# Optimization experiments

Hardware: AMD Instinct MI355X
Metric: run time of the kernel (lower is better)

Reference implementation:

```python
import jax, jax.numpy as jnp
import numpy as np

N = 50000          # num nodes
EDG = 1600000      # num edges
DIM = 128          # in_dim == out_dim (dim_h)
H = 8              # num_heads
HD = DIM // H      # head dim = 16
BN_EPS = 1e-5


def _batchnorm(x, gamma, beta):
    # training-mode BatchNorm1d: biased batch stats over node axis
    mean = x.mean(axis=0)
    var = x.var(axis=0)
    return (x - mean) * jax.lax.rsqrt(var + BN_EPS) * gamma + beta


def setup_inputs() -> dict:
    key = jax.random.key(0)
    ks = jax.random.split(key, 12)
    lin = lambda k, o, i: jax.random.normal(k, (o, i), jnp.float32) * (1.0 / np.sqrt(i))
    return {
        "h": jax.random.normal(ks[0], (N, DIM), jnp.float32),
        "edge_index": jax.random.randint(ks[1], (2, EDG), 0, N, jnp.int32),
        "edge_attr": jax.random.normal(ks[2], (EDG, DIM), jnp.float32),
        "Wq": lin(ks[3], DIM, DIM),
        "Wk": lin(ks[4], DIM, DIM),
        "Wv": lin(ks[5], DIM, DIM),
        "We": lin(ks[6], DIM, DIM),
        "Wb": lin(ks[7], H, DIM),
        "bb": jnp.zeros((H,), jnp.float32),
        "gamma1": jnp.ones((DIM,), jnp.float32),
        "beta1": jnp.zeros((DIM,), jnp.float32),
        "W1": lin(ks[8], 2 * DIM, DIM),
        "b1": jnp.zeros((2 * DIM,), jnp.float32),
        "W2": lin(ks[9], DIM, 2 * DIM),
        "b2": jnp.zeros((DIM,), jnp.float32),
        "gamma2": jnp.ones((DIM,), jnp.float32),
        "beta2": jnp.zeros((DIM,), jnp.float32),
    }


def reference(h, edge_index, edge_attr, Wq, Wk, Wv, We, Wb, bb,
              gamma1, beta1, W1, b1, W2, b2, gamma2, beta2):
    n = h.shape[0]
    src, dst = edge_index[0], edge_index[1]

    Qh = (h @ Wq.T).reshape(n, H, HD)
    Kh = (h @ Wk.T).reshape(n, H, HD)
    Vh = (h @ Wv.T).reshape(n, H, HD)
    E = (edge_attr @ We.T).reshape(-1, H, HD)          # (EDG, H, HD)
    E_bias = edge_attr @ Wb.T + bb                      # (EDG, H)

    # per-edge attention score: sum over head dim of Kh[src]*Qh[dst]*E
    score = (Kh[src] * Qh[dst] * E).sum(-1) / np.sqrt(HD) + E_bias
    score = jnp.exp(jnp.clip(score, -5.0, 5.0))         # (EDG, H)

    msg = Vh[src] * score[..., None]                    # (EDG, H, HD)
    wV = jax.ops.segment_sum(msg, dst, num_segments=n)  # (N, H, HD)
    Z = jax.ops.segment_sum(score, dst, num_segments=n) # (N, H)

    h_attn = (wV / (Z[..., None] + 1e-6)).reshape(n, DIM)
    x = h + h_attn                                      # residual
    x = _batchnorm(x, gamma1, beta1)

    ff = jax.nn.relu(x @ W1.T + b1) @ W2.T + b2
    out = _batchnorm(x + ff, gamma2, beta2)
    return out
```

## Files before the change

kernel.cpp:

```cpp
#include <hip/hip_runtime.h>
#include <math.h>

typedef __attribute__((ext_vector_type(8))) short bf16x8;
typedef __attribute__((ext_vector_type(4))) short bf16x4;
typedef __attribute__((ext_vector_type(4))) float f32x4;

static __device__ __forceinline__ unsigned short f2bf(float x){
    union{float f; unsigned u;} v; v.f = x;
    unsigned r = v.u + 0x7fffu + ((v.u >> 16) & 1u);
    return (unsigned short)(r >> 16);
}
static __device__ __forceinline__ unsigned cvtpk(float lo, float hi){
    unsigned r;
    asm("v_cvt_pk_bf16_f32 %0, %1, %2" : "=v"(r) : "v"(lo), "v"(hi));
    return r;
}
static __device__ __forceinline__ float bflo(unsigned u){
    union{unsigned x; float f;} v; v.x = u << 16; return v.f;
}
static __device__ __forceinline__ float bfhi(unsigned u){
    union{unsigned x; float f;} v; v.x = u & 0xffff0000u; return v.f;
}

__global__ __launch_bounds__(128)
void qkv_kernel(const float* __restrict__ h,
                const float* __restrict__ Wq, const float* __restrict__ Wk,
                const float* __restrict__ Wv,
                float* __restrict__ Qb, unsigned short* __restrict__ Kb16,
                unsigned short* __restrict__ Vb16)
{
    __shared__ float hl[16 * 128];
    const int t  = threadIdx.x;
    const int n0 = blockIdx.x * 16;

    const float4* hg4 = (const float4*)(h + (size_t)n0 * 128);
    float4* hl4 = (float4*)hl;
    #pragma unroll
    for (int i = 0; i < 4; ++i) hl4[i * 128 + t] = hg4[i * 128 + t];
    __syncthreads();

    #pragma unroll
    for (int m = 0; m < 3; ++m) {
        const float* W = (m == 0 ? Wq : (m == 1 ? Wk : Wv)) + t * 128;
        float acc[16];
        #pragma unroll
        for (int n = 0; n < 16; ++n) acc[n] = 0.f;
        for (int kc = 0; kc < 32; ++kc) {
            const float4 w = *(const float4*)(W + kc * 4);
            #pragma unroll
            for (int n = 0; n < 16; ++n) {
                const float4 x = *(const float4*)&hl[n * 128 + kc * 4];
                acc[n] += w.x * x.x + w.y * x.y + w.z * x.z + w.w * x.w;
            }
        }
        if (m == 0) {
            float* o = Qb + (size_t)n0 * 128 + t;
            #pragma unroll
            for (int n = 0; n < 16; ++n) o[(size_t)n * 128] = acc[n];
        } else {
            unsigned short* o = (m == 1 ? Kb16 : Vb16) + (size_t)n0 * 128 + t;
            #pragma unroll
            for (int n = 0; n < 16; ++n) o[(size_t)n * 128] = f2bf(acc[n]);
        }
    }
}

__global__ void hist_kernel(const int* __restrict__ ei, int* __restrict__ cnt, int EDG)
{
    const int stride = gridDim.x * blockDim.x;
    for (int e = blockIdx.x * blockDim.x + threadIdx.x; e < EDG; e += stride)
        atomicAdd(&cnt[ei[EDG + e]], 1);
}

__global__ __launch_bounds__(1024)
void scan_a(const int* __restrict__ cnt, int* __restrict__ bsum, int n)
{
    __shared__ int tmp[1024];
    const int t = threadIdx.x;
    const int i = blockIdx.x * 1024 + t;
    tmp[t] = (i < n) ? cnt[i] : 0;
    __syncthreads();
    for (int d = 512; d > 0; d >>= 1) {
        if (t < d) tmp[t] += tmp[t + d];
        __syncthreads();
    }
    if (t == 0) bsum[blockIdx.x] = tmp[0];
}

__global__ void scan_b(const int* __restrict__ bsum, int* __restrict__ bbase,
                       int* __restrict__ offs, int nb, int n)
{
    if (threadIdx.x == 0) {
        int run = 0;
        for (int b = 0; b < nb; ++b) { bbase[b] = run; run += bsum[b]; }
        offs[n] = run;
    }
}

__global__ __launch_bounds__(1024)
void scan_c(const int* __restrict__ cnt, const int* __restrict__ bbase,
            int* __restrict__ offs, int n)
{
    __shared__ int tmp[1024];
    const int t = threadIdx.x;
    const int i = blockIdx.x * 1024 + t;
    const int v = (i < n) ? cnt[i] : 0;
    tmp[t] = v;
    __syncthreads();
    for (int d = 1; d < 1024; d <<= 1) {
        const int a = (t >= d) ? tmp[t - d] : 0;
        __syncthreads();
        tmp[t] += a;
        __syncthreads();
    }
    if (i < n) offs[i] = bbase[blockIdx.x] + tmp[t] - v;
}

__global__ void scatter_kernel(const int* __restrict__ ei, const int* __restrict__ offs,
                               int* __restrict__ cnt, int2* __restrict__ elist, int EDG)
{
    const int stride = gridDim.x * blockDim.x;
    for (int e = blockIdx.x * blockDim.x + threadIdx.x; e < EDG; e += stride) {
        const int d = ei[EDG + e];
        const int p = atomicSub(&cnt[d], 1) - 1;
        int2 v; v.x = ei[e]; v.y = e;
        elist[offs[d] + p] = v;
    }
}

__global__ __launch_bounds__(256, 3)
void fused_attn(const float* __restrict__ eattr, const int2* __restrict__ elist,
                const int* __restrict__ offs,
                const float* __restrict__ We, const float* __restrict__ Wb,
                const float* __restrict__ bbv,
                const float* __restrict__ Qb, const unsigned short* __restrict__ Kb16,
                const unsigned short* __restrict__ Vb16, const float* __restrict__ h,
                float* __restrict__ x, float* __restrict__ stat, int N, int EDG)
{
    __shared__ unsigned short WeB[128 * 128];
    __shared__ unsigned short WbB[16 * 128];
    __shared__ float scw[4][16][8];
    __shared__ int   srw[4][16];

    const int t = threadIdx.x;
    #pragma unroll
    for (int i = 0; i < 16; ++i) {
        const int idx4 = i * 256 + t;
        const int d = idx4 >> 5, k0 = (idx4 & 31) * 4;
        const float4 wv = *(const float4*)&We[d * 128 + k0];
        bf16x4 p;
        p[0] = (short)f2bf(wv.x); p[1] = (short)f2bf(wv.y);
        p[2] = (short)f2bf(wv.z); p[3] = (short)f2bf(wv.w);
        *(bf16x4*)((char*)WeB + d * 256 + ((2 * k0) ^ ((d & 7) << 4))) = p;
    }
    #pragma unroll
    for (int i = 0; i < 8; ++i) {
        const int idx = i * 256 + t;
        const int r = idx >> 7, k = idx & 127;
        const unsigned short v = (r < 8) ? f2bf(Wb[r * 128 + k]) : (unsigned short)0;
        *(unsigned short*)((char*)WbB + r * 256 + ((2 * k) ^ ((r & 7) << 4))) = v;
    }
    __syncthreads();

    const int l = t & 63, w = t >> 6;
    const int eloc = l & 15, g4 = l >> 4;
    const int half = l >> 5, q = l & 31;
    const int hq = q >> 2;
    const int kb_l = g4 * 16;
    float bb[8];
    #pragma unroll
    for (int hh = 0; hh < 8; ++hh) bb[hh] = bbv[hh];

    float4 sA = {0.f, 0.f, 0.f, 0.f}, sQ2 = {0.f, 0.f, 0.f, 0.f};
    const int GW = gridDim.x * 4;
    for (int node = blockIdx.x * 4 + w; node < N; node += GW) {
        const int beg = offs[node], end = offs[node + 1];

        const float* qrow = Qb + (size_t)node * 128 + g4 * 4;
        float4 qv[8];
        #pragma unroll
        for (int hh = 0; hh < 8; ++hh) qv[hh] = *(const float4*)(qrow + hh * 16);

        float4 pv = {0.f, 0.f, 0.f, 0.f};
        float zz = 0.f;

        for (int base = beg; base < end; base += 16) {
            const int cnt = min(16, end - base);
            const int ii = min(base + eloc, EDG - 1);
            const int2 se = elist[ii];

            bf16x8 frv[4];
            {
                const float* ep = eattr + (size_t)se.y * 128 + g4 * 8;
                #pragma unroll
                for (int ks = 0; ks < 4; ++ks) {
                    const float4 a0 = *(const float4*)(ep + ks * 32);
                    const float4 a1 = *(const float4*)(ep + ks * 32 + 4);
                    union { unsigned u[4]; bf16x8 v; } fr;
                    fr.u[0] = cvtpk(a0.x, a0.y);
                    fr.u[1] = cvtpk(a0.z, a0.w);
                    fr.u[2] = cvtpk(a1.x, a1.y);
                    fr.u[3] = cvtpk(a1.z, a1.w);
                    frv[ks] = fr.v;
                }
            }
            const unsigned short* kr16 = Kb16 + (size_t)se.x * 128 + g4 * 4;

            f32x4 acc[8], accb;
            #pragma unroll
            for (int hh = 0; hh < 8; ++hh) acc[hh] = (f32x4){0.f, 0.f, 0.f, 0.f};
            accb = (f32x4){0.f, 0.f, 0.f, 0.f};
            #pragma unroll
            for (int ks = 0; ks < 4; ++ks) {
                const int kb = ks * 64 + kb_l;
                const bf16x8 abf = *(const bf16x8*)((char*)WbB + eloc * 256 + (kb ^ ((eloc & 7) << 4)));
                accb = __builtin_amdgcn_mfma_f32_16x16x32_bf16(abf, frv[ks], accb, 0, 0, 0);
                #pragma unroll
                for (int hh = 0; hh < 8; ++hh) {
                    const int ar = hh * 16 + eloc;
                    const bf16x8 af = *(const bf16x8*)((char*)WeB + ar * 256 + (kb ^ ((ar & 7) << 4)));
                    acc[hh] = __builtin_amdgcn_mfma_f32_16x16x32_bf16(af, frv[ks], acc[hh], 0, 0, 0);
                }
            }

            float scv[8];
            #pragma unroll
            for (int hh = 0; hh < 8; ++hh) {
                const uint2  k2 = *(const uint2*)(kr16 + hh * 16);
                const float4 qq = qv[hh];
                float m = acc[hh][0] * (bflo(k2.x) * qq.x)
                        + acc[hh][1] * (bfhi(k2.x) * qq.y)
                        + acc[hh][2] * (bflo(k2.y) * qq.z)
                        + acc[hh][3] * (bfhi(k2.y) * qq.w);
                m += __shfl_xor(m, 16);
                m += __shfl_xor(m, 32);
                const float eb = __shfl(accb[hh & 3], ((hh >> 2) << 4) | eloc);
                float sc = m * 0.25f + eb + bb[hh];
                sc = expf(fminf(fmaxf(sc, -5.f), 5.f));
                scv[hh] = (eloc < cnt) ? sc : 0.f;
            }
            if (l < 16) {
                float4 s0 = {scv[0], scv[1], scv[2], scv[3]};
                float4 s1 = {scv[4], scv[5], scv[6], scv[7]};
                *(float4*)&scw[w][l][0] = s0;
                *(float4*)&scw[w][l][4] = s1;
                srw[w][l] = se.x;
            }
            asm volatile("s_waitcnt lgkmcnt(0)" ::: "memory");
            __builtin_amdgcn_sched_barrier(0);

            int e = half;
            for (; e + 2 < cnt; e += 4) {
                const int   s0 = srw[w][e],     s1 = srw[w][e + 2];
                const float c0 = scw[w][e][hq], c1 = scw[w][e + 2][hq];
                const uint2 u0 = *(const uint2*)(Vb16 + (size_t)s0 * 128 + 4 * q);
                const uint2 u1 = *(const uint2*)(Vb16 + (size_t)s1 * 128 + 4 * q);
                pv.x += bflo(u0.x) * c0 + bflo(u1.x) * c1;
                pv.y += bfhi(u0.x) * c0 + bfhi(u1.x) * c1;
                pv.z += bflo(u0.y) * c0 + bflo(u1.y) * c1;
                pv.w += bfhi(u0.y) * c0 + bfhi(u1.y) * c1;
                zz += c0 + c1;
            }
            for (; e < cnt; e += 2) {
                const int   s0 = srw[w][e];
                const float c0 = scw[w][e][hq];
                const uint2 u0 = *(const uint2*)(Vb16 + (size_t)s0 * 128 + 4 * q);
                pv.x += bflo(u0.x) * c0; pv.y += bfhi(u0.x) * c0;
                pv.z += bflo(u0.y) * c0; pv.w += bfhi(u0.y) * c0;
                zz += c0;
            }
        }

        pv.x += __shfl_xor(pv.x, 32); pv.y += __shfl_xor(pv.y, 32);
        pv.z += __shfl_xor(pv.z, 32); pv.w += __shfl_xor(pv.w, 32);
        zz   += __shfl_xor(zz, 32);
        if (half == 0) {
            const float inv = 1.f / (zz + 1e-6f);
            const float4 hv = *(const float4*)&h[(size_t)node * 128 + 4 * q];
            float4 xv;
            xv.x = hv.x + pv.x * inv; xv.y = hv.y + pv.y * inv;
            xv.z = hv.z + pv.z * inv; xv.w = hv.w + pv.w * inv;
            *(float4*)&x[(size_t)node * 128 + 4 * q] = xv;
            sA.x += xv.x; sA.y += xv.y; sA.z += xv.z; sA.w += xv.w;
            sQ2.x += xv.x * xv.x; sQ2.y += xv.y * xv.y;
            sQ2.z += xv.z * xv.z; sQ2.w += xv.w * xv.w;
        }
    }

    __syncthreads();
    float* wbF = (float*)WbB;
    if (half == 0) {
        *(float4*)&wbF[w * 256 + 4 * q]       = sA;
        *(float4*)&wbF[w * 256 + 128 + 4 * q] = sQ2;
    }
    __syncthreads();
    if (t < 128) {
        float s = 0.f, sq2 = 0.f;
        #pragma unroll
        for (int wi = 0; wi < 4; ++wi) {
            s   += wbF[wi * 256 + t];
            sq2 += wbF[wi * 256 + 128 + t];
        }
        atomicAdd(&stat[t], s);
        atomicAdd(&stat[128 + t], sq2);
    }
}

__global__ void bn_params(const float* __restrict__ sum, const float* __restrict__ sumsq,
                          const float* __restrict__ gamma, const float* __restrict__ beta,
                          float* __restrict__ a, float* __restrict__ b, float invn)
{
    const int c = threadIdx.x;
    const float mean = sum[c] * invn;
    const float var  = sumsq[c] * invn - mean * mean;
    const float sc   = gamma[c] * rsqrtf(var + 1e-5f);
    a[c] = sc;
    b[c] = beta[c] - mean * sc;
}

__global__ __launch_bounds__(128)
void ffn_kernel(const float* __restrict__ x, const float* __restrict__ W1,
                const float* __restrict__ b1, const float* __restrict__ W2,
                const float* __restrict__ b2, const float* __restrict__ par,
                float* __restrict__ zb, float* __restrict__ stat2)
{
    __shared__ float xnl[16 * 128];
    __shared__ float hidl[16 * 256];
    const int t  = threadIdx.x;
    const int n0 = blockIdx.x * 16;

    const float4* xg4 = (const float4*)(x + (size_t)n0 * 128);
    const float4* a4  = (const float4*)par;
    const float4* bv4 = (const float4*)(par + 128);
    float4* xnl4 = (float4*)xnl;
    #pragma unroll
    for (int i = 0; i < 4; ++i) {
        const int idx = i * 128 + t;
        const float4 xv = xg4[idx];
        const float4 av = a4[idx & 31], bv = bv4[idx & 31];
        float4 r;
        r.x = xv.x * av.x + bv.x; r.y = xv.y * av.y + bv.y;
        r.z = xv.z * av.z + bv.z; r.w = xv.w * av.w + bv.w;
        xnl4[idx] = r;
    }
    __syncthreads();

    float acc0[16], acc1[16];
    #pragma unroll
    for (int n = 0; n < 16; ++n) { acc0[n] = 0.f; acc1[n] = 0.f; }
    const float* w0p = W1 + (size_t)t * 128;
    const float* w1p = W1 + (size_t)(t + 128) * 128;
    for (int kc = 0; kc < 32; ++kc) {
        const float4 w0 = *(const float4*)(w0p + kc * 4);
        const float4 w1 = *(const float4*)(w1p + kc * 4);
        #pragma unroll
        for (int n = 0; n < 16; ++n) {
            const float4 xv = *(const float4*)&xnl[n * 128 + kc * 4];
            acc0[n] += w0.x * xv.x + w0.y * xv.y + w0.z * xv.z + w0.w * xv.w;
            acc1[n] += w1.x * xv.x + w1.y * xv.y + w1.z * xv.z + w1.w * xv.w;
        }
    }
    const float bi0 = b1[t], bi1 = b1[t + 128];
    #pragma unroll
    for (int n = 0; n < 16; ++n) {
        hidl[n * 256 + t]       = fmaxf(acc0[n] + bi0, 0.f);
        hidl[n * 256 + 128 + t] = fmaxf(acc1[n] + bi1, 0.f);
    }
    __syncthreads();

    float acc2[16];
    #pragma unroll
    for (int n = 0; n < 16; ++n) acc2[n] = 0.f;
    const float* w2p = W2 + (size_t)t * 256;
    for (int kc = 0; kc < 64; ++kc) {
        const float4 w = *(const float4*)(w2p + kc * 4);
        #pragma unroll
        for (int n = 0; n < 16; ++n) {
            const float4 hv = *(const float4*)&hidl[n * 256 + kc * 4];
            acc2[n] += w.x * hv.x + w.y * hv.y + w.z * hv.z + w.w * hv.w;
        }
    }
    const float bi2 = b2[t];
    float s = 0.f, sq = 0.f;
    float* zo = zb + (size_t)n0 * 128 + t;
    #pragma unroll
    for (int n = 0; n < 16; ++n) {
        const float z = xnl[n * 128 + t] + acc2[n] + bi2;
        zo[(size_t)n * 128] = z;
        s += z; sq += z * z;
    }
    atomicAdd(&stat2[t], s);
    atomicAdd(&stat2[128 + t], sq);
}

__global__ void final_bn(const float4* __restrict__ zb, const float* __restrict__ pa,
                         const float* __restrict__ pb, float4* __restrict__ out, int total4)
{
    const float4* a4 = (const float4*)pa;
    const float4* b4 = (const float4*)pb;
    const int stride = gridDim.x * blockDim.x;
    for (int i = blockIdx.x * blockDim.x + threadIdx.x; i < total4; i += stride) {
        const float4 z = zb[i];
        const float4 a = a4[i & 31], b = b4[i & 31];
        float4 r;
        r.x = z.x * a.x + b.x; r.y = z.y * a.y + b.y;
        r.z = z.z * a.z + b.z; r.w = z.w * a.w + b.w;
        out[i] = r;
    }
}

extern "C" void kernel_launch(void* const* d_in, const int* in_sizes, int n_in,
                              void* d_out, int out_size, void* d_ws, size_t ws_size,
                              hipStream_t stream)
{
    const float* h   = (const float*)d_in[0];
    const int*   ei  = (const int*)  d_in[1];
    const float* ea  = (const float*)d_in[2];
    const float* Wq  = (const float*)d_in[3];
    const float* Wk  = (const float*)d_in[4];
    const float* Wv  = (const float*)d_in[5];
    const float* We  = (const float*)d_in[6];
    const float* Wb  = (const float*)d_in[7];
    const float* bbv = (const float*)d_in[8];
    const float* g1  = (const float*)d_in[9];
    const float* be1 = (const float*)d_in[10];
    const float* W1  = (const float*)d_in[11];
    const float* b1  = (const float*)d_in[12];
    const float* W2  = (const float*)d_in[13];
    const float* b2  = (const float*)d_in[14];
    const float* g2  = (const float*)d_in[15];
    const float* be2 = (const float*)d_in[16];
    float* out = (float*)d_out;

    const int N   = in_sizes[0] / 128;
    const int EDG = in_sizes[1] / 2;
    const int NB  = (N + 1023) / 1024;
    const size_t nd = (size_t)N * 128;
    auto al8 = [](size_t v){ return (v + 7) & ~(size_t)7; };

    float* ws = (float*)d_ws;
    const size_t Qo  = 0;
    const size_t K16 = nd;
    const size_t V16 = nd + nd / 2;
    const size_t Xo  = 2 * nd;
    const size_t ELo = 3 * nd;
    const size_t OFo = ELo + (size_t)EDG * 2;
    const size_t CUo = al8(OFo + (size_t)N + 8);
    const size_t BSo = al8(CUo + (size_t)N);
    const size_t BBo = al8(BSo + (size_t)NB);
    const size_t STo = al8(BBo + (size_t)NB);
    const size_t PAR = STo + 512;

    int*  cnt   = (int*)(ws + CUo);
    int*  offs  = (int*)(ws + OFo);
    int*  bsum  = (int*)(ws + BSo);
    int*  bbase = (int*)(ws + BBo);
    int2* elist = (int2*)(ws + ELo);
    unsigned short* kb16 = (unsigned short*)(ws + K16);
    unsigned short* vb16 = (unsigned short*)(ws + V16);

    hipMemsetAsync(cnt, 0, (size_t)N * sizeof(int), stream);
    hipMemsetAsync(ws + STo, 0, 512 * sizeof(float), stream);

    qkv_kernel<<<N / 16, 128, 0, stream>>>(h, Wq, Wk, Wv, ws + Qo, kb16, vb16);

    hist_kernel<<<1024, 256, 0, stream>>>(ei, cnt, EDG);
    scan_a<<<NB, 1024, 0, stream>>>(cnt, bsum, N);
    scan_b<<<1, 64, 0, stream>>>(bsum, bbase, offs, NB, N);
    scan_c<<<NB, 1024, 0, stream>>>(cnt, bbase, offs, N);
    scatter_kernel<<<1024, 256, 0, stream>>>(ei, offs, cnt, elist, EDG);

    fused_attn<<<1024, 256, 0, stream>>>(ea, elist, offs, We, Wb, bbv,
                                         ws + Qo, kb16, vb16, h,
                                         ws + Xo, ws + STo, N, EDG);

    bn_params<<<1, 128, 0, stream>>>(ws + STo, ws + STo + 128, g1, be1,
                                     ws + PAR, ws + PAR + 128, 1.0f / (float)N);
    ffn_kernel<<<N / 16, 128, 0, stream>>>(ws + Xo, W1, b1, W2, b2, ws + PAR,
                                           ws + Qo, ws + STo + 256);
    bn_params<<<1, 128, 0, stream>>>(ws + STo + 256, ws + STo + 384, g2, be2,
                                     ws + PAR + 256, ws + PAR + 384, 1.0f / (float)N);
    final_bn<<<1024, 256, 0, stream>>>((const float4*)(ws + Qo), ws + PAR + 256,
                                       ws + PAR + 384, (float4*)out, N * 32);
}
```

Measured before the change: 1.094 ms.

## Store Q and K as permuted bf16 and widen V gather to 16-byte loads

Q is now stored in bf16 like K, and both use a permuted column layout that matches the MFMA output fragment order. Each lane can then fetch its Q/K values with contiguous 16-byte loads instead of scattered 8-byte K loads and fp32 Q loads. The V aggregation is reorganized so each lane loads 8 bf16 values (16 bytes) per edge, with four edge groups reduced by two shuffles instead of one. This cuts gather traffic and load instruction count in the edge loop, at the cost of bf16 rounding on Q and extra cross-lane shuffles.

```diff
diff --git a/kernel.cpp b/kernel.cpp
--- a/kernel.cpp
+++ b/kernel.cpp
@@ -26,7 +26,7 @@
 void qkv_kernel(const float* __restrict__ h,
                 const float* __restrict__ Wq, const float* __restrict__ Wk,
                 const float* __restrict__ Wv,
-                float* __restrict__ Qb, unsigned short* __restrict__ Kb16,
+                unsigned short* __restrict__ Qp16, unsigned short* __restrict__ Kp16,
                 unsigned short* __restrict__ Vb16)
 {
     __shared__ float hl[16 * 128];
@@ -38,6 +38,8 @@
     #pragma unroll
     for (int i = 0; i < 4; ++i) hl4[i * 128 + t] = hg4[i * 128 + t];
     __syncthreads();
+
+    const int pt = ((t >> 2) & 3) * 32 + (t >> 4) * 4 + (t & 3);
 
     #pragma unroll
     for (int m = 0; m < 3; ++m) {
@@ -53,15 +55,12 @@
                 acc[n] += w.x * x.x + w.y * x.y + w.z * x.z + w.w * x.w;
             }
         }
-        if (m == 0) {
-            float* o = Qb + (size_t)n0 * 128 + t;
-            #pragma unroll
-            for (int n = 0; n < 16; ++n) o[(size_t)n * 128] = acc[n];
-        } else {
-            unsigned short* o = (m == 1 ? Kb16 : Vb16) + (size_t)n0 * 128 + t;
-            #pragma unroll
-            for (int n = 0; n < 16; ++n) o[(size_t)n * 128] = f2bf(acc[n]);
-        }
+        unsigned short* o;
+        if (m == 0)      o = Qp16 + (size_t)n0 * 128 + pt;
+        else if (m == 1) o = Kp16 + (size_t)n0 * 128 + pt;
+        else             o = Vb16 + (size_t)n0 * 128 + t;
+        #pragma unroll
+        for (int n = 0; n < 16; ++n) o[(size_t)n * 128] = f2bf(acc[n]);
     }
 }
 
@@ -133,7 +132,8 @@
                 const int* __restrict__ offs,
                 const float* __restrict__ We, const float* __restrict__ Wb,
                 const float* __restrict__ bbv,
-                const float* __restrict__ Qb, const unsigned short* __restrict__ Kb16,
+                const unsigned short* __restrict__ Qp16,
+                const unsigned short* __restrict__ Kp16,
                 const unsigned short* __restrict__ Vb16, const float* __restrict__ h,
                 float* __restrict__ x, float* __restrict__ stat, int N, int EDG)
 {
@@ -163,25 +163,29 @@
     __syncthreads();
 
     const int l = t & 63, w = t >> 6;
-    const int eloc = l & 15, g4 = l >> 4;
-    const int half = l >> 5, q = l & 31;
-    const int hq = q >> 2;
+    const int eloc = l & 15;
+    const int g4 = l >> 4;
     const int kb_l = g4 * 16;
-    float bb[8];
-    #pragma unroll
-    for (int hh = 0; hh < 8; ++hh) bb[hh] = bbv[hh];
-
-    float4 sA = {0.f, 0.f, 0.f, 0.f}, sQ2 = {0.f, 0.f, 0.f, 0.f};
+    const int hpv = eloc >> 1;
+
+    float sA8[8], sQ8[8];
+    #pragma unroll
+    for (int j = 0; j < 8; ++j) { sA8[j] = 0.f; sQ8[j] = 0.f; }
+
     const int GW = gridDim.x * 4;
     for (int node = blockIdx.x * 4 + w; node < N; node += GW) {
         const int beg = offs[node], end = offs[node + 1];
 
-        const float* qrow = Qb + (size_t)node * 128 + g4 * 4;
-        float4 qv[8];
-        #pragma unroll
-        for (int hh = 0; hh < 8; ++hh) qv[hh] = *(const float4*)(qrow + hh * 16);
-
-        float4 pv = {0.f, 0.f, 0.f, 0.f};
+        uint4 qu[4];
+        {
+            const unsigned short* qp = Qp16 + (size_t)node * 128 + g4 * 32;
+            #pragma unroll
+            for (int i = 0; i < 4; ++i) qu[i] = *(const uint4*)(qp + i * 8);
+        }
+
+        float pv8[8];
+        #pragma unroll
+        for (int j = 0; j < 8; ++j) pv8[j] = 0.f;
         float zz = 0.f;
 
         for (int base = beg; base < end; base += 16) {
@@ -204,7 +208,12 @@
                     frv[ks] = fr.v;
                 }
             }
-            const unsigned short* kr16 = Kb16 + (size_t)se.x * 128 + g4 * 4;
+            uint4 ku[4];
+            {
+                const unsigned short* kp = Kp16 + (size_t)se.x * 128 + g4 * 32;
+                #pragma unroll
+                for (int i = 0; i < 4; ++i) ku[i] = *(const uint4*)(kp + i * 8);
+            }
 
             f32x4 acc[8], accb;
             #pragma unroll
@@ -226,16 +235,20 @@
             float scv[8];
             #pragma unroll
             for (int hh = 0; hh < 8; ++hh) {
-                const uint2  k2 = *(const uint2*)(kr16 + hh * 16);
-                const float4 qq = qv[hh];
-                float m = acc[hh][0] * (bflo(k2.x) * qq.x)
-                        + acc[hh][1] * (bfhi(k2.x) * qq.y)
-                        + acc[hh][2] * (bflo(k2.y) * qq.z)
-                        + acc[hh][3] * (bfhi(k2.y) * qq.w);
+                const uint4 kv = ku[hh >> 1];
+                const uint4 qv = qu[hh >> 1];
+                const unsigned ka = (hh & 1) ? kv.z : kv.x;
+                const unsigned kc2 = (hh & 1) ? kv.w : kv.y;
+                const unsigned qa = (hh & 1) ? qv.z : qv.x;
+                const unsigned qc2 = (hh & 1) ? qv.w : qv.y;
+                float m = acc[hh][0] * (bflo(ka)  * bflo(qa))
+                        + acc[hh][1] * (bfhi(ka)  * bfhi(qa))
+                        + acc[hh][2] * (bflo(kc2) * bflo(qc2))
+                        + acc[hh][3] * (bfhi(kc2) * bfhi(qc2));
                 m += __shfl_xor(m, 16);
                 m += __shfl_xor(m, 32);
                 const float eb = __shfl(accb[hh & 3], ((hh >> 2) << 4) | eloc);
-                float sc = m * 0.25f + eb + bb[hh];
+                float sc = m * 0.25f + eb + bbv[hh];
                 sc = expf(fminf(fmaxf(sc, -5.f), 5.f));
                 scv[hh] = (eloc < cnt) ? sc : 0.f;
             }
@@ -249,49 +262,53 @@
             asm volatile("s_waitcnt lgkmcnt(0)" ::: "memory");
             __builtin_amdgcn_sched_barrier(0);
 
-            int e = half;
-            for (; e + 2 < cnt; e += 4) {
-                const int   s0 = srw[w][e],     s1 = srw[w][e + 2];
-                const float c0 = scw[w][e][hq], c1 = scw[w][e + 2][hq];
-                const uint2 u0 = *(const uint2*)(Vb16 + (size_t)s0 * 128 + 4 * q);
-                const uint2 u1 = *(const uint2*)(Vb16 + (size_t)s1 * 128 + 4 * q);
-                pv.x += bflo(u0.x) * c0 + bflo(u1.x) * c1;
-                pv.y += bfhi(u0.x) * c0 + bfhi(u1.x) * c1;
-                pv.z += bflo(u0.y) * c0 + bflo(u1.y) * c1;
-                pv.w += bfhi(u0.y) * c0 + bfhi(u1.y) * c1;
-                zz += c0 + c1;
-            }
-            for (; e < cnt; e += 2) {
+            for (int e = g4; e < cnt; e += 4) {
                 const int   s0 = srw[w][e];
-                const float c0 = scw[w][e][hq];
-                const uint2 u0 = *(const uint2*)(Vb16 + (size_t)s0 * 128 + 4 * q);
-                pv.x += bflo(u0.x) * c0; pv.y += bfhi(u0.x) * c0;
-                pv.z += bflo(u0.y) * c0; pv.w += bfhi(u0.y) * c0;
+                const float c0 = scw[w][e][hpv];
+                const uint4 u = *(const uint4*)(Vb16 + (size_t)s0 * 128 + eloc * 8);
+                pv8[0] += bflo(u.x) * c0; pv8[1] += bfhi(u.x) * c0;
+                pv8[2] += bflo(u.y) * c0; pv8[3] += bfhi(u.y) * c0;
+                pv8[4] += bflo(u.z) * c0; pv8[5] += bfhi(u.z) * c0;
+                pv8[6] += bflo(u.w) * c0; pv8[7] += bfhi(u.w) * c0;
                 zz += c0;
             }
         }
 
-        pv.x += __shfl_xor(pv.x, 32); pv.y += __shfl_xor(pv.y, 32);
-        pv.z += __shfl_xor(pv.z, 32); pv.w += __shfl_xor(pv.w, 32);
-        zz   += __shfl_xor(zz, 32);
-        if (half == 0) {
+        #pragma unroll
+        for (int j = 0; j < 8; ++j) {
+            pv8[j] += __shfl_xor(pv8[j], 16);
+            pv8[j] += __shfl_xor(pv8[j], 32);
+        }
+        zz += __shfl_xor(zz, 16);
+        zz += __shfl_xor(zz, 32);
+        if (g4 == 0) {
             const float inv = 1.f / (zz + 1e-6f);
-            const float4 hv = *(const float4*)&h[(size_t)node * 128 + 4 * q];
-            float4 xv;
-            xv.x = hv.x + pv.x * inv; xv.y = hv.y + pv.y * inv;
-            xv.z = hv.z + pv.z * inv; xv.w = hv.w + pv.w * inv;
-            *(float4*)&x[(size_t)node * 128 + 4 * q] = xv;
-            sA.x += xv.x; sA.y += xv.y; sA.z += xv.z; sA.w += xv.w;
-            sQ2.x += xv.x * xv.x; sQ2.y += xv.y * xv.y;
-            sQ2.z += xv.z * xv.z; sQ2.w += xv.w * xv.w;
+            const float4 h0 = *(const float4*)&h[(size_t)node * 128 + eloc * 8];
+            const float4 h1 = *(const float4*)&h[(size_t)node * 128 + eloc * 8 + 4];
+            float4 x0, x1;
+            x0.x = h0.x + pv8[0] * inv; x0.y = h0.y + pv8[1] * inv;
+            x0.z = h0.z + pv8[2] * inv; x0.w = h0.w + pv8[3] * inv;
+            x1.x = h1.x + pv8[4] * inv; x1.y = h1.y + pv8[5] * inv;
+            x1.z = h1.z + pv8[6] * inv; x1.w = h1.w + pv8[7] * inv;
+            *(float4*)&x[(size_t)node * 128 + eloc * 8]     = x0;
+            *(float4*)&x[(size_t)node * 128 + eloc * 8 + 4] = x1;
+            sA8[0] += x0.x; sA8[1] += x0.y; sA8[2] += x0.z; sA8[3] += x0.w;
+            sA8[4] += x1.x; sA8[5] += x1.y; sA8[6] += x1.z; sA8[7] += x1.w;
+            sQ8[0] += x0.x * x0.x; sQ8[1] += x0.y * x0.y;
+            sQ8[2] += x0.z * x0.z; sQ8[3] += x0.w * x0.w;
+            sQ8[4] += x1.x * x1.x; sQ8[5] += x1.y * x1.y;
+            sQ8[6] += x1.z * x1.z; sQ8[7] += x1.w * x1.w;
         }
     }
 
     __syncthreads();
     float* wbF = (float*)WbB;
-    if (half == 0) {
-        *(float4*)&wbF[w * 256 + 4 * q]       = sA;
-        *(float4*)&wbF[w * 256 + 128 + 4 * q] = sQ2;
+    if (g4 == 0) {
+        #pragma unroll
+        for (int j = 0; j < 8; ++j) {
+            wbF[w * 256 + eloc * 8 + j]       = sA8[j];
+            wbF[w * 256 + 128 + eloc * 8 + j] = sQ8[j];
+        }
     }
     __syncthreads();
     if (t < 128) {
@@ -439,11 +456,12 @@
     auto al8 = [](size_t v){ return (v + 7) & ~(size_t)7; };
 
     float* ws = (float*)d_ws;
-    const size_t Qo  = 0;
-    const size_t K16 = nd;
-    const size_t V16 = nd + nd / 2;
-    const size_t Xo  = 2 * nd;
-    const size_t ELo = 3 * nd;
+    const size_t Xo  = 0;
+    const size_t Zo  = nd;
+    const size_t Q16 = 2 * nd;
+    const size_t K16 = 2 * nd + nd / 2;
+    const size_t V16 = 3 * nd;
+    const size_t ELo = 3 * nd + nd / 2;
     const size_t OFo = ELo + (size_t)EDG * 2;
     const size_t CUo = al8(OFo + (size_t)N + 8);
     const size_t BSo = al8(CUo + (size_t)N);
@@ -456,13 +474,14 @@
     int*  bsum  = (int*)(ws + BSo);
     int*  bbase = (int*)(ws + BBo);
     int2* elist = (int2*)(ws + ELo);
-    unsigned short* kb16 = (unsigned short*)(ws + K16);
+    unsigned short* qp16 = (unsigned short*)(ws + Q16);
+    unsigned short* kp16 = (unsigned short*)(ws + K16);
     unsigned short* vb16 = (unsigned short*)(ws + V16);
 
     hipMemsetAsync(cnt, 0, (size_t)N * sizeof(int), stream);
     hipMemsetAsync(ws + STo, 0, 512 * sizeof(float), stream);
 
-    qkv_kernel<<<N / 16, 128, 0, stream>>>(h, Wq, Wk, Wv, ws + Qo, kb16, vb16);
+    qkv_kernel<<<N / 16, 128, 0, stream>>>(h, Wq, Wk, Wv, qp16, kp16, vb16);
 
     hist_kernel<<<1024, 256, 0, stream>>>(ei, cnt, EDG);
     scan_a<<<NB, 1024, 0, stream>>>(cnt, bsum, N);
@@ -471,15 +490,15 @@
     scatter_kernel<<<1024, 256, 0, stream>>>(ei, offs, cnt, elist, EDG);
 
     fused_attn<<<1024, 256, 0, stream>>>(ea, elist, offs, We, Wb, bbv,
-                                         ws + Qo, kb16, vb16, h,
+                                         qp16, kp16, vb16, h,
                                          ws + Xo, ws + STo, N, EDG);
 
     bn_params<<<1, 128, 0, stream>>>(ws + STo, ws + STo + 128, g1, be1,
                                      ws + PAR, ws + PAR + 128, 1.0f / (float)N);
     ffn_kernel<<<N / 16, 128, 0, stream>>>(ws + Xo, W1, b1, W2, b2, ws + PAR,
-                                           ws + Qo, ws + STo + 256);
+                                           ws + Zo, ws + STo + 256);
     bn_params<<<1, 128, 0, stream>>>(ws + STo + 256, ws + STo + 384, g2, be2,
                                      ws + PAR + 256, ws + PAR + 384, 1.0f / (float)N);
-    final_bn<<<1024, 256, 0, stream>>>((const float4*)(ws + Qo), ws + PAR + 256,
+    final_bn<<<1024, 256, 0, stream>>>((const float4*)(ws + Zo), ws + PAR + 256,
                                        ws + PAR + 384, (float4*)out, N * 32);
 }
```

Measured after the change: 1.205 ms. 10.1% more time.
